# Kernel optimization log

Hardware: AMD Instinct MI355X
Metric: run time of the kernel (lower is better)

## Reference

```python
import jax, jax.numpy as jnp
import numpy as np

N_NODES = 100000

def setup_inputs() -> dict:
    key = jax.random.key(0)
    ks = jax.random.split(key, 8)
    n_feat, nhid, nclass = 256, 128, 40
    n_edges = 1600000
    x = jax.random.normal(ks[0], (N_NODES, n_feat), dtype=jnp.float32)
    edge_index = jax.random.randint(ks[1], (2, n_edges), 0, N_NODES, dtype=jnp.int64)
    # Glorot-ish scaled weights
    W1 = jax.random.normal(ks[2], (n_feat, nhid), dtype=jnp.float32) / np.sqrt(n_feat)
    b1 = jnp.zeros((nhid,), dtype=jnp.float32)
    W2 = jax.random.normal(ks[3], (nhid, nhid), dtype=jnp.float32) / np.sqrt(nhid)
    b2 = jnp.zeros((nhid,), dtype=jnp.float32)
    Wc = jax.random.normal(ks[4], (nhid, nclass), dtype=jnp.float32) / np.sqrt(nhid)
    bc = jnp.zeros((nclass,), dtype=jnp.float32)
    return {"x": x, "edge_index": edge_index, "W1": W1, "b1": b1,
            "W2": W2, "b2": b2, "Wc": Wc, "bc": bc}


def _gcn_conv(x, src, dst, W, b, n_nodes):
    """PyG GCNConv: transform, then sym-normalized aggregation with self-loops.
    out_i = sum_{j in N(i) u {i}} (d_i^-1/2 d_j^-1/2) (x_j W) + b,
    where d = in-degree over A + I.
    """
    h = x @ W  # [N, out]
    ones = jnp.ones_like(dst, dtype=h.dtype)
    deg = jax.ops.segment_sum(ones, dst, num_segments=n_nodes) + 1.0  # + self loop
    dinv = jax.lax.rsqrt(deg)  # deg >= 1, always valid
    norm = dinv[src] * dinv[dst]  # [E]
    msg = h[src] * norm[:, None]  # [E, out]  (dominant gather traffic)
    agg = jax.ops.segment_sum(msg, dst, num_segments=n_nodes)
    agg = agg + h * (dinv * dinv)[:, None]  # self-loop contribution
    return agg + b


def reference(x, edge_index, W1, b1, W2, b2, Wc, bc):
    # eval mode: dropout is identity
    src, dst = edge_index[0], edge_index[1]
    n = x.shape[0]
    h = jax.nn.relu(_gcn_conv(x, src, dst, W1, b1, n))
    h = jax.nn.relu(_gcn_conv(h, src, dst, W2, b2, n))
    return h @ Wc + bc
```

## Files before the change

### kernel.cpp

```cpp
#include <hip/hip_runtime.h>
#include <hip/hip_bf16.h>
#include <hip/hip_fp16.h>
#include <type_traits>


typedef _Float16 half8 __attribute__((ext_vector_type(8)));
typedef float floatx4 __attribute__((ext_vector_type(4)));

#define EPB 8192


__device__ inline int block_incl_scan_256(int t, int* tmp) {
    int tid = threadIdx.x;
    tmp[tid] = t;
    __syncthreads();
    #pragma unroll
    for (int off = 1; off < 256; off <<= 1) {
        int v = (tid >= off) ? tmp[tid - off] : 0;
        __syncthreads();
        tmp[tid] += v;
        __syncthreads();
    }
    return tmp[tid];
}

template <int ITEMS>
__global__ __launch_bounds__(256) void k_scan1(const int* __restrict__ v,
                                               int* __restrict__ bsum, int n) {
    __shared__ int tmp[256];
    int base = blockIdx.x * (256 * ITEMS) + threadIdx.x * ITEMS;
    int t = 0;
    #pragma unroll
    for (int l = 0; l < ITEMS; ++l) {
        int i = base + l;
        t += (i < n) ? v[i] : 0;
    }
    block_incl_scan_256(t, tmp);
    if (threadIdx.x == 0) bsum[blockIdx.x] = tmp[255];
}

__global__ __launch_bounds__(256) void k_scan2(int* __restrict__ bsum, int nb) {
    __shared__ int tmp[256];
    int tid = threadIdx.x;
    int v = (tid < nb) ? bsum[tid] : 0;
    block_incl_scan_256(v, tmp);
    if (tid < nb) bsum[tid] = tid ? tmp[tid - 1] : 0;
}

template <int ITEMS>
__global__ __launch_bounds__(256) void k_scan3(const int* __restrict__ vin,
                                               const int* __restrict__ bsum,
                                               int* __restrict__ rp, int n) {
    __shared__ int tmp[256];
    int base = blockIdx.x * (256 * ITEMS) + threadIdx.x * ITEMS;
    int v[ITEMS];
    int t = 0;
    #pragma unroll
    for (int l = 0; l < ITEMS; ++l) {
        int i = base + l;
        v[l] = (i < n) ? vin[i] : 0;
        t += v[l];
    }
    block_incl_scan_256(t, tmp);
    int run = bsum[blockIdx.x] + (threadIdx.x ? tmp[threadIdx.x - 1] : 0);
    #pragma unroll
    for (int l = 0; l < ITEMS; ++l) {
        int i = base + l;
        if (i < n) rp[i] = run;
        run += v[l];
    }
}


__global__ __launch_bounds__(256) void k_histA(const int* __restrict__ dst,
                                               int* __restrict__ histM,
                                               int E, int nblk) {
    __shared__ int h[512];
    int tid = threadIdx.x;
    for (int i = tid; i < 512; i += 256) h[i] = 0;
    __syncthreads();
    int base = blockIdx.x * EPB;
    #pragma unroll 4
    for (int l = 0; l < EPB / 256; ++l) {
        int i = base + l * 256 + tid;
        if (i < E) atomicAdd(&h[dst[i] >> 8], 1);
    }
    __syncthreads();
    for (int i = tid; i < 512; i += 256)
        histM[i * nblk + blockIdx.x] = h[i];
}

__global__ __launch_bounds__(256) void k_scatterA(const int* __restrict__ src,
                                                  const int* __restrict__ dst,
                                                  const int* __restrict__ histS,
                                                  unsigned long long* __restrict__ eB,
                                                  int E, int nblk) {
    __shared__ int bse[512];
    __shared__ int cnt[512];
    int tid = threadIdx.x;
    for (int i = tid; i < 512; i += 256) {
        bse[i] = histS[i * nblk + blockIdx.x];
        cnt[i] = 0;
    }
    __syncthreads();
    int base = blockIdx.x * EPB;
    #pragma unroll 4
    for (int l = 0; l < EPB / 256; ++l) {
        int i = base + l * 256 + tid;
        if (i < E) {
            int d = dst[i];
            int s = src[i];
            int b = d >> 8;
            int r = atomicAdd(&cnt[b], 1);
            eB[bse[b] + r] = ((unsigned long long)(unsigned)d << 32) | (unsigned)s;
        }
    }
}

#define BCAP 4608
__global__ __launch_bounds__(256) void k_sortB(const unsigned long long* __restrict__ eB,
                                               const int* __restrict__ histS,
                                               int* __restrict__ srcS,
                                               int* __restrict__ rowptr,
                                               float* __restrict__ dinv,
                                               int n, int E, int nblk) {
    const int b   = blockIdx.x;
    const int tid = threadIdx.x;
    const int ni0 = b << 8;
    int s0 = histS[b * nblk];
    int s1 = (b < 511) ? histS[(b + 1) * nblk] : E;
    int cnt = s1 - s0;
    if (cnt > BCAP) cnt = BCAP;
    if (cnt == 0 && ni0 > n) return;

    __shared__ int hist[256];
    __shared__ int tmp[256];
    __shared__ int baseA[256];
    __shared__ int cntA[256];
    __shared__ int dstL[BCAP];
    __shared__ unsigned srcL[BCAP];
    __shared__ int lbA[256];

    hist[tid] = 0;
    cntA[tid] = 0;
    __syncthreads();
    for (int i = s0 + tid; i < s0 + cnt; i += 256) {
        int d = (int)(eB[i] >> 32);
        atomicAdd(&hist[d & 255], 1);
    }
    __syncthreads();
    int own  = hist[tid];
    int incl = block_incl_scan_256(own, tmp);
    baseA[tid] = incl - own;
    __syncthreads();
    for (int i = s0 + tid; i < s0 + cnt; i += 256) {
        unsigned long long v = eB[i];
        int d = (int)(v >> 32);
        int dig = d & 255;
        int r = atomicAdd(&cntA[dig], 1);
        int pos = baseA[dig] + r;
        dstL[pos] = d;
        srcL[pos] = (unsigned)v;
    }
    __syncthreads();
    for (int j = tid; j < cnt; j += 256)
        srcS[s0 + j] = (int)srcL[j];
    if (ni0 <= n) {
        int i = ni0 + tid;
        int lo = 0, hi = cnt;
        while (lo < hi) {
            int mid = (lo + hi) >> 1;
            if (dstL[mid] < i) lo = mid + 1; else hi = mid;
        }
        lbA[tid] = lo;
        __syncthreads();
        if (i <= n) {
            rowptr[i] = s0 + lo;
            if (i < n) {
                int ub = (tid < 255) ? lbA[tid + 1] : cnt;
                dinv[i] = rsqrtf((float)(ub - lo + 1));
            }
        }
    }
}

__global__ __launch_bounds__(256) void k_wcast_all(const float* __restrict__ W1,
                                                   _Float16* __restrict__ W1t,
                                                   const float* __restrict__ W2,
                                                   _Float16* __restrict__ W2t,
                                                   const float* __restrict__ Wc,
                                                   _Float16* __restrict__ Wct) {
    int i = blockIdx.x * 256 + threadIdx.x;
    if (i < 32768) {
        int c = i >> 8, k = i & 255;
        W1t[i] = (_Float16)W1[(size_t)k * 128 + c];
    } else if (i < 32768 + 16384) {
        int j = i - 32768;
        int c = j >> 7, k = j & 127;
        W2t[j] = (_Float16)W2[(size_t)k * 128 + c];
    } else if (i < 32768 + 16384 + 6144) {
        int j = i - 32768 - 16384;
        int c = j >> 7, k = j & 127;
        Wct[j] = (c < 40) ? (_Float16)Wc[(size_t)k * 40 + c] : (_Float16)0.f;
    }
}


template <int K, int BN, typename AT, typename OT>
__global__ __launch_bounds__(256) void gemm_pf(const AT* __restrict__ A,
                                               const _Float16* __restrict__ Wt,
                                               const float* __restrict__ bias,
                                               OT* __restrict__ C,
                                               int M, int N) {
    constexpr int KP = K + 8;
    constexpr int NT = BN / 16;
    constexpr int KS = K / 32;
    __shared__ __align__(16) _Float16 Bs[BN * KP];

    const int tid  = threadIdx.x;
    const int lane = tid & 63;
    const int wv   = tid >> 6;
    const int qd   = lane >> 4;
    const int ln15 = lane & 15;
    const int bm   = blockIdx.x * 64;

    int row  = bm + wv * 16 + ln15;
    int rowc = (row < M) ? row : (M - 1);

    float4 af[std::is_same<AT, float>::value ? KS : 1][2];
    half8  ah[std::is_same<AT, float>::value ? 1 : KS];
    if constexpr (std::is_same<AT, float>::value) {
        const float* p = A + (size_t)rowc * K + qd * 8;
        #pragma unroll
        for (int ks = 0; ks < KS; ++ks) {
            af[ks][0] = *(const float4*)(p + ks * 32);
            af[ks][1] = *(const float4*)(p + ks * 32 + 4);
        }
    } else {
        const _Float16* p = (const _Float16*)A + (size_t)rowc * K + qd * 8;
        #pragma unroll
        for (int ks = 0; ks < KS; ++ks)
            ah[ks] = *(const half8*)(p + ks * 32);
    }

    constexpr int TOT = BN * K / 8;
    #pragma unroll
    for (int i = 0; i < TOT / 256; ++i) {
        int idx = (i * 256 + tid) * 8;
        int col = idx / K;
        int kk  = idx % K;
        *(uint4*)&Bs[col * KP + kk] = *(const uint4*)(Wt + idx);
    }
    __syncthreads();

    floatx4 acc[NT];
    #pragma unroll
    for (int c = 0; c < NT; ++c) acc[c] = (floatx4){0.f, 0.f, 0.f, 0.f};

    #pragma unroll
    for (int ks = 0; ks < KS; ++ks) {
        half8 a;
        if constexpr (std::is_same<AT, float>::value) {
            float4 v0 = af[ks][0];
            float4 v1 = af[ks][1];
            a[0] = (_Float16)v0.x; a[1] = (_Float16)v0.y;
            a[2] = (_Float16)v0.z; a[3] = (_Float16)v0.w;
            a[4] = (_Float16)v1.x; a[5] = (_Float16)v1.y;
            a[6] = (_Float16)v1.z; a[7] = (_Float16)v1.w;
        } else {
            a = ah[ks];
        }
        #pragma unroll
        for (int c = 0; c < NT; ++c) {
            half8 b = *(const half8*)&Bs[(c * 16 + ln15) * KP + ks * 32 + qd * 8];
            acc[c] = __builtin_amdgcn_mfma_f32_16x16x32_f16(a, b, acc[c], 0, 0, 0);
        }
    }

    int baseRow = bm + wv * 16 + qd * 4;
    #pragma unroll
    for (int c = 0; c < NT; ++c) {
        int col = c * 16 + ln15;
        if constexpr (std::is_same<OT, _Float16>::value) {
            #pragma unroll
            for (int r = 0; r < 4; ++r) {
                int rr = baseRow + r;
                if (rr < M) C[(size_t)rr * N + col] = (_Float16)acc[c][r];
            }
        } else {
            float bv = (col < N && bias) ? bias[col] : 0.f;
            #pragma unroll
            for (int r = 0; r < 4; ++r) {
                int rr = baseRow + r;
                if (rr < M && col < N)
                    ((float*)C)[(size_t)rr * N + col] = acc[c][r] + bv;
            }
        }
    }
}


static __device__ __forceinline__ float2 h2f2u(unsigned int raw) {
    __half2 h = *(__half2*)&raw;
    return __half22float2(h);
}

__global__ __launch_bounds__(256) void gcn_agg(const unsigned int* __restrict__ h,
                                               const int* __restrict__ rowptr,
                                               const int* __restrict__ srcS,
                                               const float* __restrict__ dinv,
                                               const float* __restrict__ bias,
                                               unsigned int* __restrict__ out,
                                               int n, int do_relu) {
    int node = blockIdx.x * 4 + (threadIdx.x >> 6);
    if (node >= n) return;
    const int lane = threadIdx.x & 63;
    const int g    = lane >> 4;
    const int t    = lane & 15;

    const _Float16* hb = (const _Float16*)h;

    float di = dinv[node];
    int e0 = rowptr[node];
    int e1 = rowptr[node + 1];

    half8 sv = *(const half8*)(hb + (size_t)(unsigned)node * 128 + t * 8);
    const float4* b4 = (const float4*)bias;
    float4 blo = b4[t * 2 + 0];
    float4 bhi = b4[t * 2 + 1];

    float2 acc[4];
    #pragma unroll
    for (int i = 0; i < 4; ++i) acc[i] = make_float2(0.f, 0.f);

    for (int ce = e0; ce < e1; ce += 64) {
        int cnt = e1 - ce;
        cnt = (cnt < 64) ? cnt : 64;
        int colv = 0, wval = 0;
        if (lane < cnt) {
            int c = srcS[ce + lane];
            colv = c;
            wval = __float_as_int(di * dinv[c]);
        }
        #pragma unroll 2
        for (int d = 0; d < cnt; d += 4) {
            int idx = (d + g) << 2;
            int c   = __builtin_amdgcn_ds_bpermute(idx, colv);
            float w = __int_as_float(__builtin_amdgcn_ds_bpermute(idx, wval));
            const unsigned* hp = (const unsigned*)(hb + (size_t)(unsigned)c * 128 + t * 8);
            uint4 hv = *(const uint4*)hp;
            float2 u0 = h2f2u(hv.x);
            float2 u1 = h2f2u(hv.y);
            float2 u2 = h2f2u(hv.z);
            float2 u3 = h2f2u(hv.w);
            acc[0].x += u0.x * w; acc[0].y += u0.y * w;
            acc[1].x += u1.x * w; acc[1].y += u1.y * w;
            acc[2].x += u2.x * w; acc[2].y += u2.y * w;
            acc[3].x += u3.x * w; acc[3].y += u3.y * w;
        }
    }

    #pragma unroll
    for (int i = 0; i < 4; ++i) {
        acc[i].x += __shfl_xor(acc[i].x, 16);
        acc[i].y += __shfl_xor(acc[i].y, 16);
        acc[i].x += __shfl_xor(acc[i].x, 32);
        acc[i].y += __shfl_xor(acc[i].y, 32);
    }

    float s = di * di;
    float bb[8] = {blo.x, blo.y, blo.z, blo.w, bhi.x, bhi.y, bhi.z, bhi.w};
    half8 o;
    #pragma unroll
    for (int i = 0; i < 8; ++i) {
        float v = ((i & 1) ? acc[i >> 1].y : acc[i >> 1].x) + (float)sv[i] * s + bb[i];
        if (do_relu) v = fmaxf(v, 0.f);
        o[i] = (_Float16)v;
    }
    if (g == 0)
        *(half8*)((_Float16*)out + (size_t)(unsigned)node * 128 + t * 8) = o;
}


extern "C" void kernel_launch(void* const* d_in, const int* in_sizes, int n_in,
                              void* d_out, int out_size, void* d_ws, size_t ws_size,
                              hipStream_t stream) {
    const float* x  = (const float*)d_in[0];
    const int* eidx = (const int*)d_in[1];
    const float* W1 = (const float*)d_in[2];
    const float* b1 = (const float*)d_in[3];
    const float* W2 = (const float*)d_in[4];
    const float* b2 = (const float*)d_in[5];
    const float* Wc = (const float*)d_in[6];
    const float* bc = (const float*)d_in[7];
    float* out = (float*)d_out;

    const int NF = 256, NH = 128, NC = 40;
    const int n = in_sizes[0] / NF;
    const int E = in_sizes[1] / 2;
    const int* src = eidx;
    const int* dst = eidx + E;

    const int nblk = (E + EPB - 1) / EPB;
    const int hm   = 512 * nblk;
    const int nbA  = (hm + 4095) / 4096;

    char* wsb = (char*)d_ws;
    size_t off = 0;
    auto alloc = [&](size_t bytes) {
        char* p = wsb + off;
        off = (off + bytes + 511) & ~(size_t)511;
        return p;
    };
    _Float16* hbuf = (_Float16*)alloc((size_t)n * NH * 2);
    _Float16* abuf = (_Float16*)alloc((size_t)n * NH * 2);
    _Float16* W1t  = (_Float16*)alloc((size_t)128 * 256 * 2);
    _Float16* W2t  = (_Float16*)alloc((size_t)128 * 128 * 2);
    _Float16* Wct  = (_Float16*)alloc((size_t)48 * 128 * 2);
    unsigned long long* eB = (unsigned long long*)alloc((size_t)E * 8);
    int* srcS      = (int*)alloc((size_t)E * 4);
    int* histM     = (int*)alloc((size_t)hm * 4);
    int* histS     = (int*)alloc((size_t)hm * 4);
    int* rowptr    = (int*)alloc((size_t)(n + 1) * 4);
    float* dinv    = (float*)alloc((size_t)n * 4);
    int* bsumA     = (int*)alloc(1024);

    k_histA<<<nblk, 256, 0, stream>>>(dst, histM, E, nblk);
    k_scan1<16><<<nbA, 256, 0, stream>>>(histM, bsumA, hm);
    k_scan2<<<1, 256, 0, stream>>>(bsumA, nbA);
    k_scan3<16><<<nbA, 256, 0, stream>>>(histM, bsumA, histS, hm);
    k_scatterA<<<nblk, 256, 0, stream>>>(src, dst, histS, eB, E, nblk);
    k_sortB<<<512, 256, 0, stream>>>(eB, histS, srcS, rowptr, dinv, n, E, nblk);

    k_wcast_all<<<(32768 + 16384 + 6144 + 255) / 256, 256, 0, stream>>>(
        W1, W1t, W2, W2t, Wc, Wct);

    const int gB = (n + 63) / 64;
    gemm_pf<256, 128, float, _Float16><<<gB, 256, 0, stream>>>(x, W1t, nullptr, hbuf, n, NH);
    gcn_agg<<<(n + 3) / 4, 256, 0, stream>>>((const unsigned int*)hbuf, rowptr, srcS, dinv, b1,
                                             (unsigned int*)abuf, n, 1);
    gemm_pf<128, 128, _Float16, _Float16><<<gB, 256, 0, stream>>>(abuf, W2t, nullptr, hbuf, n, NH);
    gcn_agg<<<(n + 3) / 4, 256, 0, stream>>>((const unsigned int*)hbuf, rowptr, srcS, dinv, b2,
                                             (unsigned int*)abuf, n, 1);
    gemm_pf<128, 48, _Float16, float><<<gB, 256, 0, stream>>>(abuf, Wct, bc, out, n, NC);
}
```

Baseline: 394.8 us.

## Use finer 1024-bucket CSR sort and fuse scan passes

Node buckets for the two-pass radix CSR build shrink from 256 to 128 nodes, so k_sortB runs 1024 blocks with smaller shared buffers (short dst digits, BCAP 2560), which should raise occupancy. The separate block-sum scan kernel is removed: each k_scan3f block rescans the block sums itself, saving one launch. The aggregation also clamps source indices to n-1. The trade-offs are a larger histogram matrix and a tighter per-bucket capacity that could truncate edges if a bucket receives more than 2560.

```diff
diff --git a/kernel.cpp b/kernel.cpp
--- a/kernel.cpp
+++ b/kernel.cpp
@@ -8,6 +8,8 @@
 typedef float floatx4 __attribute__((ext_vector_type(4)));
 
 #define EPB 8192
+#define NBKT 1024
+#define BCAP 2560
 
 
 __device__ inline int block_incl_scan_256(int t, int* tmp) {
@@ -39,20 +41,18 @@
     if (threadIdx.x == 0) bsum[blockIdx.x] = tmp[255];
 }
 
-__global__ __launch_bounds__(256) void k_scan2(int* __restrict__ bsum, int nb) {
+template <int ITEMS>
+__global__ __launch_bounds__(256) void k_scan3f(const int* __restrict__ vin,
+                                                const int* __restrict__ bsum,
+                                                int* __restrict__ rp, int n, int nb) {
     __shared__ int tmp[256];
     int tid = threadIdx.x;
-    int v = (tid < nb) ? bsum[tid] : 0;
-    block_incl_scan_256(v, tmp);
-    if (tid < nb) bsum[tid] = tid ? tmp[tid - 1] : 0;
-}
-
-template <int ITEMS>
-__global__ __launch_bounds__(256) void k_scan3(const int* __restrict__ vin,
-                                               const int* __restrict__ bsum,
-                                               int* __restrict__ rp, int n) {
-    __shared__ int tmp[256];
-    int base = blockIdx.x * (256 * ITEMS) + threadIdx.x * ITEMS;
+    int bs = (tid < nb && tid < (int)blockIdx.x) ? bsum[tid] : 0;
+    block_incl_scan_256(bs, tmp);
+    int base0 = tmp[255];
+    __syncthreads();
+
+    int base = blockIdx.x * (256 * ITEMS) + tid * ITEMS;
     int v[ITEMS];
     int t = 0;
     #pragma unroll
@@ -61,8 +61,8 @@
         v[l] = (i < n) ? vin[i] : 0;
         t += v[l];
     }
-    block_incl_scan_256(t, tmp);
-    int run = bsum[blockIdx.x] + (threadIdx.x ? tmp[threadIdx.x - 1] : 0);
+    int incl = block_incl_scan_256(t, tmp);
+    int run = base0 + incl - t;
     #pragma unroll
     for (int l = 0; l < ITEMS; ++l) {
         int i = base + l;
@@ -75,18 +75,18 @@
 __global__ __launch_bounds__(256) void k_histA(const int* __restrict__ dst,
                                                int* __restrict__ histM,
                                                int E, int nblk) {
-    __shared__ int h[512];
+    __shared__ int h[NBKT];
     int tid = threadIdx.x;
-    for (int i = tid; i < 512; i += 256) h[i] = 0;
+    for (int i = tid; i < NBKT; i += 256) h[i] = 0;
     __syncthreads();
     int base = blockIdx.x * EPB;
     #pragma unroll 4
     for (int l = 0; l < EPB / 256; ++l) {
         int i = base + l * 256 + tid;
-        if (i < E) atomicAdd(&h[dst[i] >> 8], 1);
-    }
-    __syncthreads();
-    for (int i = tid; i < 512; i += 256)
+        if (i < E) atomicAdd(&h[dst[i] >> 7], 1);
+    }
+    __syncthreads();
+    for (int i = tid; i < NBKT; i += 256)
         histM[i * nblk + blockIdx.x] = h[i];
 }
 
@@ -95,10 +95,10 @@
                                                   const int* __restrict__ histS,
                                                   unsigned long long* __restrict__ eB,
                                                   int E, int nblk) {
-    __shared__ int bse[512];
-    __shared__ int cnt[512];
+    __shared__ int bse[NBKT];
+    __shared__ int cnt[NBKT];
     int tid = threadIdx.x;
-    for (int i = tid; i < 512; i += 256) {
+    for (int i = tid; i < NBKT; i += 256) {
         bse[i] = histS[i * nblk + blockIdx.x];
         cnt[i] = 0;
     }
@@ -110,14 +110,13 @@
         if (i < E) {
             int d = dst[i];
             int s = src[i];
-            int b = d >> 8;
+            int b = d >> 7;
             int r = atomicAdd(&cnt[b], 1);
             eB[bse[b] + r] = ((unsigned long long)(unsigned)d << 32) | (unsigned)s;
         }
     }
 }
 
-#define BCAP 4608
 __global__ __launch_bounds__(256) void k_sortB(const unsigned long long* __restrict__ eB,
                                                const int* __restrict__ histS,
                                                int* __restrict__ srcS,
@@ -126,9 +125,9 @@
                                                int n, int E, int nblk) {
     const int b   = blockIdx.x;
     const int tid = threadIdx.x;
-    const int ni0 = b << 8;
+    const int ni0 = b << 7;
     int s0 = histS[b * nblk];
-    int s1 = (b < 511) ? histS[(b + 1) * nblk] : E;
+    int s1 = (b < NBKT - 1) ? histS[(b + 1) * nblk] : E;
     int cnt = s1 - s0;
     if (cnt > BCAP) cnt = BCAP;
     if (cnt == 0 && ni0 > n) return;
@@ -137,17 +136,15 @@
     __shared__ int tmp[256];
     __shared__ int baseA[256];
     __shared__ int cntA[256];
-    __shared__ int dstL[BCAP];
+    __shared__ short dstL[BCAP];
     __shared__ unsigned srcL[BCAP];
-    __shared__ int lbA[256];
+    __shared__ int lbA[128];
 
     hist[tid] = 0;
     cntA[tid] = 0;
     __syncthreads();
-    for (int i = s0 + tid; i < s0 + cnt; i += 256) {
-        int d = (int)(eB[i] >> 32);
-        atomicAdd(&hist[d & 255], 1);
-    }
+    for (int i = s0 + tid; i < s0 + cnt; i += 256)
+        atomicAdd(&hist[(int)(eB[i] >> 32) & 127], 1);
     __syncthreads();
     int own  = hist[tid];
     int incl = block_incl_scan_256(own, tmp);
@@ -155,30 +152,34 @@
     __syncthreads();
     for (int i = s0 + tid; i < s0 + cnt; i += 256) {
         unsigned long long v = eB[i];
-        int d = (int)(v >> 32);
-        int dig = d & 255;
+        int dig = (int)(v >> 32) & 127;
         int r = atomicAdd(&cntA[dig], 1);
         int pos = baseA[dig] + r;
-        dstL[pos] = d;
+        dstL[pos] = (short)dig;
         srcL[pos] = (unsigned)v;
     }
     __syncthreads();
     for (int j = tid; j < cnt; j += 256)
         srcS[s0 + j] = (int)srcL[j];
     if (ni0 <= n) {
-        int i = ni0 + tid;
-        int lo = 0, hi = cnt;
-        while (lo < hi) {
-            int mid = (lo + hi) >> 1;
-            if (dstL[mid] < i) lo = mid + 1; else hi = mid;
-        }
-        lbA[tid] = lo;
+        if (tid < 128) {
+            int lo = 0, hi = cnt;
+            while (lo < hi) {
+                int mid = (lo + hi) >> 1;
+                if ((int)dstL[mid] < tid) lo = mid + 1; else hi = mid;
+            }
+            lbA[tid] = lo;
+        }
         __syncthreads();
-        if (i <= n) {
-            rowptr[i] = s0 + lo;
-            if (i < n) {
-                int ub = (tid < 255) ? lbA[tid + 1] : cnt;
-                dinv[i] = rsqrtf((float)(ub - lo + 1));
+        if (tid < 128) {
+            int i = ni0 + tid;
+            if (i <= n) {
+                int lo = lbA[tid];
+                rowptr[i] = s0 + lo;
+                if (i < n) {
+                    int ub = (tid < 127) ? lbA[tid + 1] : cnt;
+                    dinv[i] = rsqrtf((float)(ub - lo + 1));
+                }
             }
         }
     }
@@ -333,13 +334,15 @@
     #pragma unroll
     for (int i = 0; i < 4; ++i) acc[i] = make_float2(0.f, 0.f);
 
+    const unsigned nclamp = (unsigned)n - 1u;
     for (int ce = e0; ce < e1; ce += 64) {
         int cnt = e1 - ce;
         cnt = (cnt < 64) ? cnt : 64;
         int colv = 0, wval = 0;
         if (lane < cnt) {
-            int c = srcS[ce + lane];
-            colv = c;
+            unsigned c = (unsigned)srcS[ce + lane];
+            c = (c < nclamp) ? c : nclamp;
+            colv = (int)c;
             wval = __float_as_int(di * dinv[c]);
         }
         #pragma unroll 2
@@ -402,7 +405,7 @@
     const int* dst = eidx + E;
 
     const int nblk = (E + EPB - 1) / EPB;
-    const int hm   = 512 * nblk;
+    const int hm   = NBKT * nblk;
     const int nbA  = (hm + 4095) / 4096;
 
     char* wsb = (char*)d_ws;
@@ -427,10 +430,9 @@
 
     k_histA<<<nblk, 256, 0, stream>>>(dst, histM, E, nblk);
     k_scan1<16><<<nbA, 256, 0, stream>>>(histM, bsumA, hm);
-    k_scan2<<<1, 256, 0, stream>>>(bsumA, nbA);
-    k_scan3<16><<<nbA, 256, 0, stream>>>(histM, bsumA, histS, hm);
+    k_scan3f<16><<<nbA, 256, 0, stream>>>(histM, bsumA, histS, hm, nbA);
     k_scatterA<<<nblk, 256, 0, stream>>>(src, dst, histS, eB, E, nblk);
-    k_sortB<<<512, 256, 0, stream>>>(eB, histS, srcS, rowptr, dinv, n, E, nblk);
+    k_sortB<<<NBKT, 256, 0, stream>>>(eB, histS, srcS, rowptr, dinv, n, E, nblk);
 
     k_wcast_all<<<(32768 + 16384 + 6144 + 255) / 256, 256, 0, stream>>>(
         W1, W1t, W2, W2t, Wc, Wct);
```

Result: no change. 399.1 us (+1.1%).
